# Performance work log

Hardware: AMD Instinct MI355X
Metric: run time of the kernel (lower is better)

Reference implementation:

```python
import jax, jax.numpy as jnp
import numpy as np

B, N = 32, 64
ATTR, STATE, REL, GDIM = 4, 8, 4, 32
NF = 128

def _ln(x, w, b, eps=1e-5):
    mu = jnp.mean(x, axis=-1, keepdims=True)
    var = jnp.mean((x - mu) ** 2, axis=-1, keepdims=True)
    return (x - mu) * jax.lax.rsqrt(var + eps) * w + b

def setup_inputs() -> dict:
    key = jax.random.key(0)
    ks = iter(jax.random.split(key, 32))
    d = {}
    d['attrs'] = jax.random.normal(next(ks), (B, N, ATTR), jnp.float32)
    d['states'] = jax.random.normal(next(ks), (B, N, STATE), jnp.float32)
    d['actions'] = jnp.zeros((B, N, 4), jnp.float32)  # action=False, unused
    d['rel_attrs'] = jax.random.normal(next(ks), (B, N, N, REL), jnp.float32)
    def w(shape):
        return jax.random.normal(next(ks), shape, jnp.float32) * 0.05
    d['oe_w0'] = w((NF, ATTR + STATE)); d['oe_b0'] = jnp.zeros((NF,), jnp.float32)
    d['oe_w1'] = w((NF, NF));            d['oe_b1'] = jnp.zeros((NF,), jnp.float32)
    d['re_w0'] = w((NF, STATE + REL + 2 * ATTR)); d['re_b0'] = jnp.zeros((NF,), jnp.float32)
    d['re_w1'] = w((NF, NF));            d['re_b1'] = jnp.zeros((NF,), jnp.float32)
    d['rp_w'] = w((NF, NF + 2 * NF));    d['rp_b'] = jnp.zeros((NF,), jnp.float32)
    d['rp_lnw'] = jnp.ones((NF,), jnp.float32); d['rp_lnb'] = jnp.zeros((NF,), jnp.float32)
    d['pp_w'] = w((NF, 2 * NF));         d['pp_b'] = jnp.zeros((NF,), jnp.float32)
    d['pp_lnw'] = jnp.ones((NF,), jnp.float32); d['pp_lnb'] = jnp.zeros((NF,), jnp.float32)
    d['pr_w0'] = w((NF, NF));            d['pr_b0'] = jnp.zeros((NF,), jnp.float32)
    d['pr_w1'] = w((GDIM, NF));          d['pr_b1'] = jnp.zeros((GDIM,), jnp.float32)
    d['pstep'] = 2
    return d

def reference(attrs, states, actions, rel_attrs,
              oe_w0, oe_b0, oe_w1, oe_b1,
              re_w0, re_b0, re_w1, re_b1,
              rp_w, rp_b, rp_lnw, rp_lnb,
              pp_w, pp_b, pp_lnw, pp_lnb,
              pr_w0, pr_b0, pr_w1, pr_b1, pstep):
    lin = lambda x, w, b: jnp.einsum('...i,oi->...o', x, w) + b
    # ---- encode nodes: [B,N,attr+state] -> [B,N,NF] (action=False) ----
    obj_in = jnp.concatenate([attrs, states], axis=2)
    obj_encode = jax.nn.relu(lin(jax.nn.relu(lin(obj_in, oe_w0, oe_b0)), oe_w1, oe_b1))
    # ---- encode edges over dense N x N pairs ----
    rel_states = states[:, :, None, :] - states[:, None, :, :]        # B,N,N,state
    recv_attr = jnp.broadcast_to(attrs[:, :, None, :], (attrs.shape[0], attrs.shape[1], attrs.shape[1], attrs.shape[2]))
    send_attr = jnp.broadcast_to(attrs[:, None, :, :], recv_attr.shape)
    rel_in = jnp.concatenate([rel_attrs, rel_states, recv_attr, send_attr], axis=3)
    rel_encode = jax.nn.relu(lin(jax.nn.relu(lin(rel_in, re_w0, re_b0)), re_w1, re_b1))  # B,N,N,NF
    # ---- propagation steps ----
    for _ in range(pstep):
        sh = rel_encode.shape[:3] + (obj_encode.shape[-1],)
        recv = jnp.broadcast_to(obj_encode[:, :, None, :], sh)
        send = jnp.broadcast_to(obj_encode[:, None, :, :], sh)
        rel_effect = jax.nn.relu(_ln(lin(jnp.concatenate([rel_encode, recv, send], axis=3), rp_w, rp_b), rp_lnw, rp_lnb))
        rel_agg = rel_effect.sum(axis=2)                               # B,N,NF
        obj_encode = jax.nn.relu(_ln(lin(jnp.concatenate([obj_encode, rel_agg], axis=2), pp_w, pp_b), pp_lnw, pp_lnb))
    # ---- predict + tanh (state_encoder has tanh=True) ----
    out = lin(jax.nn.relu(lin(obj_encode, pr_w0, pr_b0)), pr_w1, pr_b1)
    return jnp.tanh(out)
```

## Files before the change

kernel.cpp:

```cpp
#include <hip/hip_runtime.h>


#define ROWS 2048
typedef unsigned short u16;
typedef unsigned int u32;
typedef __attribute__((ext_vector_type(8))) short bf16x8;
typedef __attribute__((ext_vector_type(4))) float f32x4;

__device__ __forceinline__ u16 f2b(float f) {
    u32 u = __float_as_uint(f);
    u32 r = (u + 0x7fffu + ((u >> 16) & 1u)) >> 16;
    return (u16)r;
}

__global__ __launch_bounds__(256)
void k_prep(const float* __restrict__ re_w1, const float* __restrict__ rp_w,
            const float* __restrict__ oe_w1, const float* __restrict__ pp_w,
            const float* __restrict__ pr_w0, const float* __restrict__ pr_w1,
            u16* __restrict__ wbfA, u16* __restrict__ wbfB,
            u16* __restrict__ oe_w1b, u16* __restrict__ wrecvb, u16* __restrict__ wsendb,
            u16* __restrict__ pp_wb, u16* __restrict__ pr_w0b, u16* __restrict__ pr_w1b)
{
    int idx = blockIdx.x * 256 + threadIdx.x;
    if (idx < 18432) { int r = idx / 144, c = idx - r * 144;
        wbfA[idx] = f2b(c < 128 ? re_w1[r * 128 + c] : 0.f); return; }
    idx -= 18432;
    if (idx < 18432) { int r = idx / 144, c = idx - r * 144;
        wbfB[idx] = f2b(c < 128 ? rp_w[r * 384 + c] : 0.f); return; }
    idx -= 18432;
    if (idx < 16384) { oe_w1b[idx] = f2b(oe_w1[idx]); return; }
    idx -= 16384;
    if (idx < 16384) { int r = idx >> 7, c = idx & 127;
        wrecvb[idx] = f2b(rp_w[r * 384 + 128 + c]); return; }
    idx -= 16384;
    if (idx < 16384) { int r = idx >> 7, c = idx & 127;
        wsendb[idx] = f2b(rp_w[r * 384 + 256 + c]); return; }
    idx -= 16384;
    if (idx < 32768) { pp_wb[idx] = f2b(pp_w[idx]); return; }
    idx -= 32768;
    if (idx < 16384) { pr_w0b[idx] = f2b(pr_w0[idx]); return; }
    idx -= 16384;
    if (idx < 4096)  { pr_w1b[idx] = f2b(pr_w1[idx]); }
}

__global__ __launch_bounds__(256)
void k_node(const float* __restrict__ attrs, const float* __restrict__ states,
            const float* __restrict__ oe_w0, const float* __restrict__ oe_b0,
            const u16* __restrict__ oe_w1b, const float* __restrict__ oe_b1,
            const float* __restrict__ re_w0, const float* __restrict__ re_b0,
            const u16* __restrict__ wrecvb, const u16* __restrict__ wsendb,
            const float* __restrict__ rp_b,
            u16* __restrict__ objb, float* __restrict__ nr, float* __restrict__ ns,
            float* __restrict__ recvT, float* __restrict__ sendT)
{
    const int r0 = blockIdx.x * 16;
    const int t = threadIdx.x;
    __shared__ float xs[16][12];
    __shared__ float w0s[1536];
    __shared__ float rw0s[2560];
    __shared__ __align__(16) u16 hb[16 * 136];
    __shared__ __align__(16) u16 ob[16 * 136];

    if (t < 192) { int row = t / 12, c = t - row * 12;
        xs[row][c] = (c < 4) ? attrs[(r0 + row) * 4 + c] : states[(r0 + row) * 8 + (c - 4)]; }
    for (int i = t; i < 1536; i += 256) w0s[i] = oe_w0[i];
    for (int i = t; i < 2560; i += 256) rw0s[i] = re_w0[i];
    __syncthreads();

    for (int e = t; e < 2048; e += 256) {
        int row = e >> 7, o = e & 127;
        float h = oe_b0[o];
#pragma unroll
        for (int k = 0; k < 12; k++) h += w0s[o * 12 + k] * xs[row][k];
        hb[row * 136 + o] = f2b(fmaxf(h, 0.f));
        float s0 = 0.f, a0 = 0.f, a1 = 0.f;
#pragma unroll
        for (int k = 0; k < 8; k++) s0 += rw0s[o * 20 + 4 + k] * xs[row][4 + k];
#pragma unroll
        for (int k = 0; k < 4; k++) {
            a0 += rw0s[o * 20 + 12 + k] * xs[row][k];
            a1 += rw0s[o * 20 + 16 + k] * xs[row][k];
        }
        nr[(r0 + row) * 128 + o] = s0 + a0 + re_b0[o];
        ns[(r0 + row) * 128 + o] = a1 - s0;
    }
    __syncthreads();

    const int wave = t >> 6, lane = t & 63, tx = lane & 15, quad = lane >> 4;

    bf16x8 afr[4];
#pragma unroll
    for (int kk = 0; kk < 4; kk++) afr[kk] = *(const bf16x8*)&hb[tx * 136 + kk * 32 + quad * 8];
    f32x4 acc[2]; acc[0] = (f32x4){0.f,0.f,0.f,0.f}; acc[1] = acc[0];
#pragma unroll
    for (int ot = 0; ot < 2; ot++) {
        int o = (wave * 2 + ot) * 16 + tx;
#pragma unroll
        for (int kk = 0; kk < 4; kk++) {
            bf16x8 bfr = *(const bf16x8*)&oe_w1b[o * 128 + kk * 32 + quad * 8];
            acc[ot] = __builtin_amdgcn_mfma_f32_16x16x32_bf16(afr[kk], bfr, acc[ot], 0, 0, 0);
        }
    }
#pragma unroll
    for (int ot = 0; ot < 2; ot++) {
        int o = (wave * 2 + ot) * 16 + tx;
        float bia = oe_b1[o];
#pragma unroll
        for (int r = 0; r < 4; r++)
            ob[(quad * 4 + r) * 136 + o] = f2b(fmaxf(acc[ot][r] + bia, 0.f));
    }
    __syncthreads();
    { int m = t >> 4, c = t & 15;
      *(uint4*)&objb[(r0 + m) * 128 + c * 8] = *(const uint4*)&ob[m * 136 + c * 8]; }

#pragma unroll
    for (int kk = 0; kk < 4; kk++) afr[kk] = *(const bf16x8*)&ob[tx * 136 + kk * 32 + quad * 8];
    f32x4 ar[2], an[2];
    ar[0] = (f32x4){0.f,0.f,0.f,0.f}; ar[1] = ar[0]; an[0] = ar[0]; an[1] = ar[0];
#pragma unroll
    for (int ot = 0; ot < 2; ot++) {
        int o = (wave * 2 + ot) * 16 + tx;
#pragma unroll
        for (int kk = 0; kk < 4; kk++) {
            bf16x8 br = *(const bf16x8*)&wrecvb[o * 128 + kk * 32 + quad * 8];
            ar[ot] = __builtin_amdgcn_mfma_f32_16x16x32_bf16(afr[kk], br, ar[ot], 0, 0, 0);
            bf16x8 bs = *(const bf16x8*)&wsendb[o * 128 + kk * 32 + quad * 8];
            an[ot] = __builtin_amdgcn_mfma_f32_16x16x32_bf16(afr[kk], bs, an[ot], 0, 0, 0);
        }
    }
#pragma unroll
    for (int ot = 0; ot < 2; ot++) {
        int o = (wave * 2 + ot) * 16 + tx;
        float rb = rp_b[o];
#pragma unroll
        for (int r = 0; r < 4; r++) {
            recvT[(r0 + quad * 4 + r) * 128 + o] = ar[ot][r] + rb;
            sendT[(r0 + quad * 4 + r) * 128 + o] = an[ot][r];
        }
    }
}

__global__ __launch_bounds__(256)
void k_edge_enc(const float* __restrict__ rel_attrs,
                const float* __restrict__ re_w0, const u16* __restrict__ wbf,
                const float* __restrict__ re_b1,
                const float* __restrict__ nr, const float* __restrict__ ns,
                u16* __restrict__ relEF)
{
    const int t = threadIdx.x;
    __shared__ __align__(16) u16 wlds[128 * 144];
    __shared__ __align__(16) u16 hsb[64 * 144];
    __shared__ float nrs[128];
    __shared__ float w0a[128][4];
    __shared__ float ras[64][4];

    {
        const uint4* src = (const uint4*)wbf;
        uint4* dst = (uint4*)wlds;
        for (int i = t; i < 2304; i += 256) dst[i] = src[i];
    }
    if (t < 128) {
#pragma unroll
        for (int c = 0; c < 4; c++) w0a[t][c] = re_w0[t * 20 + c];
    }
    const int wave = t >> 6, lane = t & 63, tx = lane & 15, quad = lane >> 4;

    for (int g = 0; g < 4; g++) {
        const int blkg = blockIdx.x * 4 + g;
        const int b = blkg >> 6;
        __syncthreads();
        if (t < 128) nrs[t] = nr[blkg * 128 + t];
        else if (t < 192) {
            int j = t - 128;
#pragma unroll
            for (int c = 0; c < 4; c++) ras[j][c] = rel_attrs[(blkg * 64 + j) * 4 + c];
        }
        __syncthreads();

        for (int e = t; e < 64 * 128; e += 256) {
            int j = e >> 7, o = e & 127;
            float v = nrs[o] + ns[(b * 64 + j) * 128 + o];
#pragma unroll
            for (int c = 0; c < 4; c++) v += w0a[o][c] * ras[j][c];
            hsb[j * 144 + o] = f2b(fmaxf(v, 0.f));
        }
        __syncthreads();

        bf16x8 afr[4];
#pragma unroll
        for (int kk = 0; kk < 4; kk++)
            afr[kk] = *(const bf16x8*)&hsb[(wave * 16 + tx) * 144 + kk * 32 + quad * 8];

        f32x4 acc[8];
#pragma unroll
        for (int oo = 0; oo < 8; oo++) acc[oo] = (f32x4){0.f, 0.f, 0.f, 0.f};
#pragma unroll
        for (int oo = 0; oo < 8; oo++) {
            const int o = oo * 16 + tx;
#pragma unroll
            for (int kk = 0; kk < 4; kk++) {
                bf16x8 bfr = *(const bf16x8*)&wlds[o * 144 + kk * 32 + quad * 8];
                acc[oo] = __builtin_amdgcn_mfma_f32_16x16x32_bf16(afr[kk], bfr, acc[oo], 0, 0, 0);
            }
        }
        __syncthreads();

#pragma unroll
        for (int oo = 0; oo < 8; oo++) {
            const int o = oo * 16 + tx;
            float bia = re_b1[o];
#pragma unroll
            for (int r = 0; r < 4; r++)
                hsb[(wave * 16 + quad * 4 + r) * 144 + o] = f2b(fmaxf(acc[oo][r] + bia, 0.f));
        }
#pragma unroll
        for (int kt = 0; kt < 4; kt++) {
            bf16x8 v = *(const bf16x8*)&hsb[(wave * 16 + tx) * 144 + kt * 32 + quad * 8];
            *(bf16x8*)(relEF + ((size_t)((blkg * 4 + wave) * 4 + kt) * 64 + lane) * 8) = v;
        }
    }
}

__global__ __launch_bounds__(256)
void k_prop_edge(const u16* __restrict__ relEF, const u16* __restrict__ wbf,
                 const float* __restrict__ rp_lnw, const float* __restrict__ rp_lnb,
                 const float* __restrict__ recvT, const float* __restrict__ sendT,
                 u16* __restrict__ aggb)
{
    const int t = threadIdx.x;
    __shared__ __align__(16) u16 wlds[128 * 144];
    __shared__ float scr[16 * 132];
    __shared__ float lnws[128], lnbs[128];

    {
        const uint4* src = (const uint4*)wbf;
        uint4* dst = (uint4*)wlds;
        for (int i = t; i < 2304; i += 256) dst[i] = src[i];
    }
    if (t < 128) { lnws[t] = rp_lnw[t]; lnbs[t] = rp_lnb[t]; }
    __syncthreads();

    const int wave = t >> 6, lane = t & 63, tx = lane & 15, quad = lane >> 4;

    for (int g = 0; g < 4; g++) {
        const int blkg = blockIdx.x * 4 + g;
        const int b = blkg >> 6;

        bf16x8 afr[4];
#pragma unroll
        for (int kt = 0; kt < 4; kt++)
            afr[kt] = *(const bf16x8*)(relEF + ((size_t)((blkg * 4 + wave) * 4 + kt) * 64 + lane) * 8);

        f32x4 acc[8];
#pragma unroll
        for (int oo = 0; oo < 8; oo++) acc[oo] = (f32x4){0.f, 0.f, 0.f, 0.f};
#pragma unroll
        for (int oo = 0; oo < 8; oo++) {
            const int o = oo * 16 + tx;
#pragma unroll
            for (int kk = 0; kk < 4; kk++) {
                bf16x8 bfr = *(const bf16x8*)&wlds[o * 144 + kk * 32 + quad * 8];
                acc[oo] = __builtin_amdgcn_mfma_f32_16x16x32_bf16(afr[kk], bfr, acc[oo], 0, 0, 0);
            }
        }

        const int jrow = wave * 16 + quad * 4;
#pragma unroll
        for (int oo = 0; oo < 8; oo++) {
            const int o = oo * 16 + tx;
            float rv = recvT[blkg * 128 + o];
#pragma unroll
            for (int r = 0; r < 4; r++)
                acc[oo][r] += rv + sendT[(b * 64 + jrow + r) * 128 + o];
        }

        float s[4], q[4];
#pragma unroll
        for (int r = 0; r < 4; r++) {
            s[r] = 0.f; q[r] = 0.f;
#pragma unroll
            for (int oo = 0; oo < 8; oo++) { s[r] += acc[oo][r]; q[r] += acc[oo][r] * acc[oo][r]; }
        }
#pragma unroll
        for (int m = 1; m < 16; m <<= 1) {
#pragma unroll
            for (int r = 0; r < 4; r++) {
                s[r] += __shfl_xor(s[r], m, 64);
                q[r] += __shfl_xor(q[r], m, 64);
            }
        }
        float mu[4], rs[4];
#pragma unroll
        for (int r = 0; r < 4; r++) {
            mu[r] = s[r] * (1.f / 128.f);
            float var = q[r] * (1.f / 128.f) - mu[r] * mu[r];
            rs[r] = rsqrtf(var + 1e-5f);
        }

        float pa[8];
#pragma unroll
        for (int oo = 0; oo < 8; oo++) {
            const int o = oo * 16 + tx;
            float lw = lnws[o], lb = lnbs[o];
            float p = 0.f;
#pragma unroll
            for (int r = 0; r < 4; r++) {
                float z = (acc[oo][r] - mu[r]) * rs[r] * lw + lb;
                p += fmaxf(z, 0.f);
            }
            pa[oo] = p;
        }
        __syncthreads();
        const int grp = wave * 4 + quad;
#pragma unroll
        for (int oo = 0; oo < 8; oo++) scr[grp * 132 + oo * 16 + tx] = pa[oo];
        __syncthreads();
        if (t < 128) {
            float sum = 0.f;
#pragma unroll
            for (int gg = 0; gg < 16; gg++) sum += scr[gg * 132 + t];
            aggb[blkg * 128 + t] = f2b(sum);
        }
    }
}

__global__ __launch_bounds__(256)
void k_prop_node(const u16* __restrict__ aggb,
                 const u16* __restrict__ pp_wb, const float* __restrict__ pp_b,
                 const float* __restrict__ pp_lnw, const float* __restrict__ pp_lnb,
                 const u16* __restrict__ wrecvb, const u16* __restrict__ wsendb,
                 const float* __restrict__ rp_b,
                 u16* __restrict__ objb, float* __restrict__ recvT, float* __restrict__ sendT,
                 int compute_terms)
{
    const int r0 = blockIdx.x * 16;
    const int t = threadIdx.x;
    __shared__ __align__(16) u16 ab[16 * 264];
    __shared__ __align__(16) u16 ob[16 * 136];
    __shared__ float redS[64], redQ[64];

    for (int i = t; i < 512; i += 256) {
        int m = i >> 5, c = i & 31;
        uint4 v = (c < 16) ? *(const uint4*)&objb[(r0 + m) * 128 + (c & 15) * 8]
                           : *(const uint4*)&aggb[(r0 + m) * 128 + (c - 16) * 8];
        *(uint4*)&ab[m * 264 + c * 8] = v;
    }
    __syncthreads();

    const int wave = t >> 6, lane = t & 63, tx = lane & 15, quad = lane >> 4;
    bf16x8 afr[8];
#pragma unroll
    for (int kk = 0; kk < 8; kk++) afr[kk] = *(const bf16x8*)&ab[tx * 264 + kk * 32 + quad * 8];
    f32x4 acc[2]; acc[0] = (f32x4){0.f,0.f,0.f,0.f}; acc[1] = acc[0];
#pragma unroll
    for (int ot = 0; ot < 2; ot++) {
        int o = (wave * 2 + ot) * 16 + tx;
#pragma unroll
        for (int kk = 0; kk < 8; kk++) {
            bf16x8 bfr = *(const bf16x8*)&pp_wb[o * 256 + kk * 32 + quad * 8];
            acc[ot] = __builtin_amdgcn_mfma_f32_16x16x32_bf16(afr[kk], bfr, acc[ot], 0, 0, 0);
        }
    }
#pragma unroll
    for (int ot = 0; ot < 2; ot++) {
        float bia = pp_b[(wave * 2 + ot) * 16 + tx];
#pragma unroll
        for (int r = 0; r < 4; r++) acc[ot][r] += bia;
    }

    float s[4], q[4];
#pragma unroll
    for (int r = 0; r < 4; r++) {
        s[r] = acc[0][r] + acc[1][r];
        q[r] = acc[0][r] * acc[0][r] + acc[1][r] * acc[1][r];
    }
#pragma unroll
    for (int m = 1; m < 16; m <<= 1) {
#pragma unroll
        for (int r = 0; r < 4; r++) {
            s[r] += __shfl_xor(s[r], m, 64);
            q[r] += __shfl_xor(q[r], m, 64);
        }
    }
    if (tx == 0) {
#pragma unroll
        for (int r = 0; r < 4; r++) {
            redS[wave * 16 + quad * 4 + r] = s[r];
            redQ[wave * 16 + quad * 4 + r] = q[r];
        }
    }
    __syncthreads();
    float mu[4], rs[4];
#pragma unroll
    for (int r = 0; r < 4; r++) {
        int m = quad * 4 + r;
        float ss = redS[m] + redS[16 + m] + redS[32 + m] + redS[48 + m];
        float qq = redQ[m] + redQ[16 + m] + redQ[32 + m] + redQ[48 + m];
        mu[r] = ss * (1.f / 128.f);
        rs[r] = rsqrtf(qq * (1.f / 128.f) - mu[r] * mu[r] + 1e-5f);
    }
#pragma unroll
    for (int ot = 0; ot < 2; ot++) {
        int o = (wave * 2 + ot) * 16 + tx;
        float lw = pp_lnw[o], lb = pp_lnb[o];
#pragma unroll
        for (int r = 0; r < 4; r++) {
            float z = (acc[ot][r] - mu[r]) * rs[r] * lw + lb;
            ob[(quad * 4 + r) * 136 + o] = f2b(fmaxf(z, 0.f));
        }
    }
    __syncthreads();
    { int m = t >> 4, c = t & 15;
      *(uint4*)&objb[(r0 + m) * 128 + c * 8] = *(const uint4*)&ob[m * 136 + c * 8]; }

    if (compute_terms) {
        bf16x8 af2[4];
#pragma unroll
        for (int kk = 0; kk < 4; kk++) af2[kk] = *(const bf16x8*)&ob[tx * 136 + kk * 32 + quad * 8];
        f32x4 ar[2], an[2];
        ar[0] = (f32x4){0.f,0.f,0.f,0.f}; ar[1] = ar[0]; an[0] = ar[0]; an[1] = ar[0];
#pragma unroll
        for (int ot = 0; ot < 2; ot++) {
            int o = (wave * 2 + ot) * 16 + tx;
#pragma unroll
            for (int kk = 0; kk < 4; kk++) {
                bf16x8 br = *(const bf16x8*)&wrecvb[o * 128 + kk * 32 + quad * 8];
                ar[ot] = __builtin_amdgcn_mfma_f32_16x16x32_bf16(af2[kk], br, ar[ot], 0, 0, 0);
                bf16x8 bs = *(const bf16x8*)&wsendb[o * 128 + kk * 32 + quad * 8];
                an[ot] = __builtin_amdgcn_mfma_f32_16x16x32_bf16(af2[kk], bs, an[ot], 0, 0, 0);
            }
        }
#pragma unroll
        for (int ot = 0; ot < 2; ot++) {
            int o = (wave * 2 + ot) * 16 + tx;
            float rb = rp_b[o];
#pragma unroll
            for (int r = 0; r < 4; r++) {
                recvT[(r0 + quad * 4 + r) * 128 + o] = ar[ot][r] + rb;
                sendT[(r0 + quad * 4 + r) * 128 + o] = an[ot][r];
            }
        }
    }
}

__global__ __launch_bounds__(256)
void k_predict(const u16* __restrict__ objb,
               const u16* __restrict__ pr_w0b, const float* __restrict__ pr_b0,
               const u16* __restrict__ pr_w1b, const float* __restrict__ pr_b1,
               float* __restrict__ out)
{
    const int r0 = blockIdx.x * 16;
    const int t = threadIdx.x;
    __shared__ __align__(16) u16 ab[16 * 136];
    __shared__ __align__(16) u16 hb2[16 * 136];
    { int m = t >> 4, c = t & 15;
      *(uint4*)&ab[m * 136 + c * 8] = *(const uint4*)&objb[(r0 + m) * 128 + c * 8]; }
    __syncthreads();

    const int wave = t >> 6, lane = t & 63, tx = lane & 15, quad = lane >> 4;
    bf16x8 afr[4];
#pragma unroll
    for (int kk = 0; kk < 4; kk++) afr[kk] = *(const bf16x8*)&ab[tx * 136 + kk * 32 + quad * 8];
    f32x4 acc[2]; acc[0] = (f32x4){0.f,0.f,0.f,0.f}; acc[1] = acc[0];
#pragma unroll
    for (int ot = 0; ot < 2; ot++) {
        int o = (wave * 2 + ot) * 16 + tx;
#pragma unroll
        for (int kk = 0; kk < 4; kk++) {
            bf16x8 bfr = *(const bf16x8*)&pr_w0b[o * 128 + kk * 32 + quad * 8];
            acc[ot] = __builtin_amdgcn_mfma_f32_16x16x32_bf16(afr[kk], bfr, acc[ot], 0, 0, 0);
        }
    }
#pragma unroll
    for (int ot = 0; ot < 2; ot++) {
        int o = (wave * 2 + ot) * 16 + tx;
        float bia = pr_b0[o];
#pragma unroll
        for (int r = 0; r < 4; r++)
            hb2[(quad * 4 + r) * 136 + o] = f2b(fmaxf(acc[ot][r] + bia, 0.f));
    }
    __syncthreads();
    if (wave < 2) {
        bf16x8 af2[4];
#pragma unroll
        for (int kk = 0; kk < 4; kk++) af2[kk] = *(const bf16x8*)&hb2[tx * 136 + kk * 32 + quad * 8];
        f32x4 a2 = (f32x4){0.f,0.f,0.f,0.f};
        int o = wave * 16 + tx;
#pragma unroll
        for (int kk = 0; kk < 4; kk++) {
            bf16x8 bfr = *(const bf16x8*)&pr_w1b[o * 128 + kk * 32 + quad * 8];
            a2 = __builtin_amdgcn_mfma_f32_16x16x32_bf16(af2[kk], bfr, a2, 0, 0, 0);
        }
        float bia = pr_b1[o];
#pragma unroll
        for (int r = 0; r < 4; r++)
            out[(r0 + quad * 4 + r) * 32 + o] = tanhf(a2[r] + bia);
    }
}

extern "C" void kernel_launch(void* const* d_in, const int* in_sizes, int n_in,
                              void* d_out, int out_size, void* d_ws, size_t ws_size,
                              hipStream_t stream)
{
    const float* attrs    = (const float*)d_in[0];
    const float* states   = (const float*)d_in[1];
    const float* rel_attrs= (const float*)d_in[3];
    const float* oe_w0 = (const float*)d_in[4];
    const float* oe_b0 = (const float*)d_in[5];
    const float* oe_w1 = (const float*)d_in[6];
    const float* oe_b1 = (const float*)d_in[7];
    const float* re_w0 = (const float*)d_in[8];
    const float* re_b0 = (const float*)d_in[9];
    const float* re_w1 = (const float*)d_in[10];
    const float* re_b1 = (const float*)d_in[11];
    const float* rp_w  = (const float*)d_in[12];
    const float* rp_b  = (const float*)d_in[13];
    const float* rp_lnw= (const float*)d_in[14];
    const float* rp_lnb= (const float*)d_in[15];
    const float* pp_w  = (const float*)d_in[16];
    const float* pp_b  = (const float*)d_in[17];
    const float* pp_lnw= (const float*)d_in[18];
    const float* pp_lnb= (const float*)d_in[19];
    const float* pr_w0 = (const float*)d_in[20];
    const float* pr_b0 = (const float*)d_in[21];
    const float* pr_w1 = (const float*)d_in[22];
    const float* pr_b1 = (const float*)d_in[23];

    float* ws    = (float*)d_ws;
    float* nr    = ws;
    float* ns    = nr    + ROWS * 128;
    float* recvT = ns    + ROWS * 128;
    float* sendT = recvT + ROWS * 128;
    u16* wbfA   = (u16*)(sendT + ROWS * 128);
    u16* wbfB   = wbfA + 18432;
    u16* oe_w1b = wbfB + 18432;
    u16* wrecvb = oe_w1b + 16384;
    u16* wsendb = wrecvb + 16384;
    u16* pp_wb  = wsendb + 16384;
    u16* pr_w0b = pp_wb + 32768;
    u16* pr_w1b = pr_w0b + 16384;
    u16* objb   = pr_w1b + 4096;
    u16* aggb   = objb + ROWS * 128;
    u16* relEF  = aggb + ROWS * 128;

    k_prep<<<544, 256, 0, stream>>>(re_w1, rp_w, oe_w1, pp_w, pr_w0, pr_w1,
                                    wbfA, wbfB, oe_w1b, wrecvb, wsendb,
                                    pp_wb, pr_w0b, pr_w1b);
    k_node<<<128, 256, 0, stream>>>(attrs, states, oe_w0, oe_b0, oe_w1b, oe_b1,
                                    re_w0, re_b0, wrecvb, wsendb, rp_b,
                                    objb, nr, ns, recvT, sendT);
    k_edge_enc<<<512, 256, 0, stream>>>(rel_attrs, re_w0, wbfA, re_b1, nr, ns, relEF);
    for (int p = 0; p < 2; p++) {
        k_prop_edge<<<512, 256, 0, stream>>>(relEF, wbfB, rp_lnw, rp_lnb, recvT, sendT, aggb);
        k_prop_node<<<128, 256, 0, stream>>>(aggb, pp_wb, pp_b, pp_lnw, pp_lnb,
                                             wrecvb, wsendb, rp_b,
                                             objb, recvT, sendT, (p == 0) ? 1 : 0);
    }
    k_predict<<<128, 256, 0, stream>>>(objb, pr_w0b, pr_b0, pr_w1b, pr_b1, (float*)d_out);
}
```

Measured before the change: 199.6 us.

## Fuse edge encoder with first propagation GEMM and cache rel-effect product

The edge encoder and the first propagation step are merged into one kernel. It computes rel_encode·Wrel in registers and stores that loop-invariant product as bf16, in place of the rel_encode features. The second propagation step then runs a GEMM-free kernel that reads the cached product, adds the recv/send terms, and applies LayerNorm, ReLU and the sum. This removes one kernel launch, one relEF round trip and a repeated 128x128 GEMM over all edges. In exchange, the second step uses a bf16-rounded pre-activation, and the fused kernel reads its second weight matrix straight from global memory instead of LDS.

```diff
diff --git a/kernel.cpp b/kernel.cpp
--- a/kernel.cpp
+++ b/kernel.cpp
@@ -5,8 +5,10 @@
 typedef unsigned short u16;
 typedef unsigned int u32;
 typedef __attribute__((ext_vector_type(8))) short bf16x8;
+typedef __attribute__((ext_vector_type(4))) short bf16x4;
 typedef __attribute__((ext_vector_type(4))) float f32x4;
 
+__device__ __forceinline__ float bsu(u16 u) { return __uint_as_float(((u32)u) << 16); }
 __device__ __forceinline__ u16 f2b(float f) {
     u32 u = __float_as_uint(f);
     u32 r = (u + 0x7fffu + ((u >> 16) & 1u)) >> 16;
@@ -17,17 +19,16 @@
 void k_prep(const float* __restrict__ re_w1, const float* __restrict__ rp_w,
             const float* __restrict__ oe_w1, const float* __restrict__ pp_w,
             const float* __restrict__ pr_w0, const float* __restrict__ pr_w1,
-            u16* __restrict__ wbfA, u16* __restrict__ wbfB,
+            u16* __restrict__ re_w1b, u16* __restrict__ web,
             u16* __restrict__ oe_w1b, u16* __restrict__ wrecvb, u16* __restrict__ wsendb,
             u16* __restrict__ pp_wb, u16* __restrict__ pr_w0b, u16* __restrict__ pr_w1b)
 {
     int idx = blockIdx.x * 256 + threadIdx.x;
-    if (idx < 18432) { int r = idx / 144, c = idx - r * 144;
-        wbfA[idx] = f2b(c < 128 ? re_w1[r * 128 + c] : 0.f); return; }
-    idx -= 18432;
-    if (idx < 18432) { int r = idx / 144, c = idx - r * 144;
-        wbfB[idx] = f2b(c < 128 ? rp_w[r * 384 + c] : 0.f); return; }
-    idx -= 18432;
+    if (idx < 16384) { re_w1b[idx] = f2b(re_w1[idx]); return; }
+    idx -= 16384;
+    if (idx < 16384) { int r = idx >> 7, c = idx & 127;
+        web[idx] = f2b(rp_w[r * 384 + c]); return; }
+    idx -= 16384;
     if (idx < 16384) { oe_w1b[idx] = f2b(oe_w1[idx]); return; }
     idx -= 16384;
     if (idx < 16384) { int r = idx >> 7, c = idx & 127;
@@ -141,11 +142,13 @@
 }
 
 __global__ __launch_bounds__(256)
-void k_edge_enc(const float* __restrict__ rel_attrs,
-                const float* __restrict__ re_w0, const u16* __restrict__ wbf,
-                const float* __restrict__ re_b1,
-                const float* __restrict__ nr, const float* __restrict__ ns,
-                u16* __restrict__ relEF)
+void k_edge_fused(const float* __restrict__ rel_attrs,
+                  const float* __restrict__ re_w0, const u16* __restrict__ re_w1b,
+                  const u16* __restrict__ web, const float* __restrict__ re_b1,
+                  const float* __restrict__ rp_lnw, const float* __restrict__ rp_lnb,
+                  const float* __restrict__ nr, const float* __restrict__ ns,
+                  const float* __restrict__ recvT, const float* __restrict__ sendT,
+                  u16* __restrict__ Ebuf, u16* __restrict__ aggb)
 {
     const int t = threadIdx.x;
     __shared__ __align__(16) u16 wlds[128 * 144];
@@ -153,13 +156,17 @@
     __shared__ float nrs[128];
     __shared__ float w0a[128][4];
     __shared__ float ras[64][4];
+    __shared__ float scr[16 * 132];
+    __shared__ float lnws[128], lnbs[128];
 
     {
-        const uint4* src = (const uint4*)wbf;
-        uint4* dst = (uint4*)wlds;
-        for (int i = t; i < 2304; i += 256) dst[i] = src[i];
+        for (int i = t; i < 2048; i += 256) {
+            int r = i >> 4, c8 = i & 15;
+            *(uint4*)&wlds[r * 144 + c8 * 8] = *(const uint4*)&re_w1b[r * 128 + c8 * 8];
+        }
     }
     if (t < 128) {
+        lnws[t] = rp_lnw[t]; lnbs[t] = rp_lnb[t];
 #pragma unroll
         for (int c = 0; c < 4; c++) w0a[t][c] = re_w0[t * 20 + c];
     }
@@ -190,7 +197,6 @@
 #pragma unroll
         for (int kk = 0; kk < 4; kk++)
             afr[kk] = *(const bf16x8*)&hsb[(wave * 16 + tx) * 144 + kk * 32 + quad * 8];
-
         f32x4 acc[8];
 #pragma unroll
         for (int oo = 0; oo < 8; oo++) acc[oo] = (f32x4){0.f, 0.f, 0.f, 0.f};
@@ -203,8 +209,6 @@
                 acc[oo] = __builtin_amdgcn_mfma_f32_16x16x32_bf16(afr[kk], bfr, acc[oo], 0, 0, 0);
             }
         }
-        __syncthreads();
-
 #pragma unroll
         for (int oo = 0; oo < 8; oo++) {
             const int o = oo * 16 + tx;
@@ -213,55 +217,29 @@
             for (int r = 0; r < 4; r++)
                 hsb[(wave * 16 + quad * 4 + r) * 144 + o] = f2b(fmaxf(acc[oo][r] + bia, 0.f));
         }
-#pragma unroll
-        for (int kt = 0; kt < 4; kt++) {
-            bf16x8 v = *(const bf16x8*)&hsb[(wave * 16 + tx) * 144 + kt * 32 + quad * 8];
-            *(bf16x8*)(relEF + ((size_t)((blkg * 4 + wave) * 4 + kt) * 64 + lane) * 8) = v;
-        }
-    }
-}
-
-__global__ __launch_bounds__(256)
-void k_prop_edge(const u16* __restrict__ relEF, const u16* __restrict__ wbf,
-                 const float* __restrict__ rp_lnw, const float* __restrict__ rp_lnb,
-                 const float* __restrict__ recvT, const float* __restrict__ sendT,
-                 u16* __restrict__ aggb)
-{
-    const int t = threadIdx.x;
-    __shared__ __align__(16) u16 wlds[128 * 144];
-    __shared__ float scr[16 * 132];
-    __shared__ float lnws[128], lnbs[128];
-
-    {
-        const uint4* src = (const uint4*)wbf;
-        uint4* dst = (uint4*)wlds;
-        for (int i = t; i < 2304; i += 256) dst[i] = src[i];
-    }
-    if (t < 128) { lnws[t] = rp_lnw[t]; lnbs[t] = rp_lnb[t]; }
-    __syncthreads();
-
-    const int wave = t >> 6, lane = t & 63, tx = lane & 15, quad = lane >> 4;
-
-    for (int g = 0; g < 4; g++) {
-        const int blkg = blockIdx.x * 4 + g;
-        const int b = blkg >> 6;
-
-        bf16x8 afr[4];
-#pragma unroll
-        for (int kt = 0; kt < 4; kt++)
-            afr[kt] = *(const bf16x8*)(relEF + ((size_t)((blkg * 4 + wave) * 4 + kt) * 64 + lane) * 8);
-
-        f32x4 acc[8];
-#pragma unroll
-        for (int oo = 0; oo < 8; oo++) acc[oo] = (f32x4){0.f, 0.f, 0.f, 0.f};
+        bf16x8 af2[4];
+#pragma unroll
+        for (int kk = 0; kk < 4; kk++)
+            af2[kk] = *(const bf16x8*)&hsb[(wave * 16 + tx) * 144 + kk * 32 + quad * 8];
+        f32x4 acc2[8];
+#pragma unroll
+        for (int oo = 0; oo < 8; oo++) acc2[oo] = (f32x4){0.f, 0.f, 0.f, 0.f};
 #pragma unroll
         for (int oo = 0; oo < 8; oo++) {
-            const int o = oo * 16 + tx;
+            const int o2 = oo * 16 + tx;
 #pragma unroll
             for (int kk = 0; kk < 4; kk++) {
-                bf16x8 bfr = *(const bf16x8*)&wlds[o * 144 + kk * 32 + quad * 8];
-                acc[oo] = __builtin_amdgcn_mfma_f32_16x16x32_bf16(afr[kk], bfr, acc[oo], 0, 0, 0);
+                bf16x8 bfr = *(const bf16x8*)&web[o2 * 128 + kk * 32 + quad * 8];
+                acc2[oo] = __builtin_amdgcn_mfma_f32_16x16x32_bf16(af2[kk], bfr, acc2[oo], 0, 0, 0);
             }
+        }
+        const int tid = blkg * 4 + wave;
+#pragma unroll
+        for (int oo = 0; oo < 8; oo++) {
+            bf16x4 v;
+            v[0] = (short)f2b(acc2[oo][0]); v[1] = (short)f2b(acc2[oo][1]);
+            v[2] = (short)f2b(acc2[oo][2]); v[3] = (short)f2b(acc2[oo][3]);
+            *(bf16x4*)(Ebuf + ((size_t)(tid * 8 + oo) * 64 + lane) * 4) = v;
         }
 
         const int jrow = wave * 16 + quad * 4;
@@ -271,15 +249,14 @@
             float rv = recvT[blkg * 128 + o];
 #pragma unroll
             for (int r = 0; r < 4; r++)
-                acc[oo][r] += rv + sendT[(b * 64 + jrow + r) * 128 + o];
-        }
-
+                acc2[oo][r] += rv + sendT[(b * 64 + jrow + r) * 128 + o];
+        }
         float s[4], q[4];
 #pragma unroll
         for (int r = 0; r < 4; r++) {
             s[r] = 0.f; q[r] = 0.f;
 #pragma unroll
-            for (int oo = 0; oo < 8; oo++) { s[r] += acc[oo][r]; q[r] += acc[oo][r] * acc[oo][r]; }
+            for (int oo = 0; oo < 8; oo++) { s[r] += acc2[oo][r]; q[r] += acc2[oo][r] * acc2[oo][r]; }
         }
 #pragma unroll
         for (int m = 1; m < 16; m <<= 1) {
@@ -296,7 +273,6 @@
             float var = q[r] * (1.f / 128.f) - mu[r] * mu[r];
             rs[r] = rsqrtf(var + 1e-5f);
         }
-
         float pa[8];
 #pragma unroll
         for (int oo = 0; oo < 8; oo++) {
@@ -305,7 +281,7 @@
             float p = 0.f;
 #pragma unroll
             for (int r = 0; r < 4; r++) {
-                float z = (acc[oo][r] - mu[r]) * rs[r] * lw + lb;
+                float z = (acc2[oo][r] - mu[r]) * rs[r] * lw + lb;
                 p += fmaxf(z, 0.f);
             }
             pa[oo] = p;
@@ -321,6 +297,80 @@
             for (int gg = 0; gg < 16; gg++) sum += scr[gg * 132 + t];
             aggb[blkg * 128 + t] = f2b(sum);
         }
+    }
+}
+
+__global__ __launch_bounds__(256)
+void k_prop_edge2(const u16* __restrict__ Ebuf,
+                  const float* __restrict__ rp_lnw, const float* __restrict__ rp_lnb,
+                  const float* __restrict__ recvT, const float* __restrict__ sendT,
+                  u16* __restrict__ aggb)
+{
+    const int blk = blockIdx.x;
+    const int b = blk >> 6;
+    const int t = threadIdx.x;
+    __shared__ float scr[16 * 132];
+    __shared__ float lnws[128], lnbs[128];
+    if (t < 128) { lnws[t] = rp_lnw[t]; lnbs[t] = rp_lnb[t]; }
+    __syncthreads();
+
+    const int wave = t >> 6, lane = t & 63, tx = lane & 15, quad = lane >> 4;
+    const int tid = blk * 4 + wave;
+    const int jrow = wave * 16 + quad * 4;
+
+    float y[8][4];
+#pragma unroll
+    for (int oo = 0; oo < 8; oo++) {
+        bf16x4 v = *(const bf16x4*)(Ebuf + ((size_t)(tid * 8 + oo) * 64 + lane) * 4);
+        const int o = oo * 16 + tx;
+        float rv = recvT[blk * 128 + o];
+#pragma unroll
+        for (int r = 0; r < 4; r++)
+            y[oo][r] = bsu((u16)v[r]) + rv + sendT[(b * 64 + jrow + r) * 128 + o];
+    }
+    float s[4], q[4];
+#pragma unroll
+    for (int r = 0; r < 4; r++) {
+        s[r] = 0.f; q[r] = 0.f;
+#pragma unroll
+        for (int oo = 0; oo < 8; oo++) { s[r] += y[oo][r]; q[r] += y[oo][r] * y[oo][r]; }
+    }
+#pragma unroll
+    for (int m = 1; m < 16; m <<= 1) {
+#pragma unroll
+        for (int r = 0; r < 4; r++) {
+            s[r] += __shfl_xor(s[r], m, 64);
+            q[r] += __shfl_xor(q[r], m, 64);
+        }
+    }
+    float mu[4], rs[4];
+#pragma unroll
+    for (int r = 0; r < 4; r++) {
+        mu[r] = s[r] * (1.f / 128.f);
+        rs[r] = rsqrtf(q[r] * (1.f / 128.f) - mu[r] * mu[r] + 1e-5f);
+    }
+    float pa[8];
+#pragma unroll
+    for (int oo = 0; oo < 8; oo++) {
+        const int o = oo * 16 + tx;
+        float lw = lnws[o], lb = lnbs[o];
+        float p = 0.f;
+#pragma unroll
+        for (int r = 0; r < 4; r++) {
+            float z = (y[oo][r] - mu[r]) * rs[r] * lw + lb;
+            p += fmaxf(z, 0.f);
+        }
+        pa[oo] = p;
+    }
+    const int grp = wave * 4 + quad;
+#pragma unroll
+    for (int oo = 0; oo < 8; oo++) scr[grp * 132 + oo * 16 + tx] = pa[oo];
+    __syncthreads();
+    if (t < 128) {
+        float sum = 0.f;
+#pragma unroll
+        for (int gg = 0; gg < 16; gg++) sum += scr[gg * 132 + t];
+        aggb[blk * 128 + t] = f2b(sum);
     }
 }
 
@@ -531,30 +581,33 @@
     float* ns    = nr    + ROWS * 128;
     float* recvT = ns    + ROWS * 128;
     float* sendT = recvT + ROWS * 128;
-    u16* wbfA   = (u16*)(sendT + ROWS * 128);
-    u16* wbfB   = wbfA + 18432;
-    u16* oe_w1b = wbfB + 18432;
+    u16* re_w1b = (u16*)(sendT + ROWS * 128);
+    u16* web    = re_w1b + 16384;
+    u16* oe_w1b = web    + 16384;
     u16* wrecvb = oe_w1b + 16384;
     u16* wsendb = wrecvb + 16384;
     u16* pp_wb  = wsendb + 16384;
-    u16* pr_w0b = pp_wb + 32768;
+    u16* pr_w0b = pp_wb  + 32768;
     u16* pr_w1b = pr_w0b + 16384;
     u16* objb   = pr_w1b + 4096;
     u16* aggb   = objb + ROWS * 128;
-    u16* relEF  = aggb + ROWS * 128;
-
-    k_prep<<<544, 256, 0, stream>>>(re_w1, rp_w, oe_w1, pp_w, pr_w0, pr_w1,
-                                    wbfA, wbfB, oe_w1b, wrecvb, wsendb,
+    u16* Ebuf   = aggb + ROWS * 128;
+
+    k_prep<<<528, 256, 0, stream>>>(re_w1, rp_w, oe_w1, pp_w, pr_w0, pr_w1,
+                                    re_w1b, web, oe_w1b, wrecvb, wsendb,
                                     pp_wb, pr_w0b, pr_w1b);
     k_node<<<128, 256, 0, stream>>>(attrs, states, oe_w0, oe_b0, oe_w1b, oe_b1,
                                     re_w0, re_b0, wrecvb, wsendb, rp_b,
                                     objb, nr, ns, recvT, sendT);
-    k_edge_enc<<<512, 256, 0, stream>>>(rel_attrs, re_w0, wbfA, re_b1, nr, ns, relEF);
-    for (int p = 0; p < 2; p++) {
-        k_prop_edge<<<512, 256, 0, stream>>>(relEF, wbfB, rp_lnw, rp_lnb, recvT, sendT, aggb);
-        k_prop_node<<<128, 256, 0, stream>>>(aggb, pp_wb, pp_b, pp_lnw, pp_lnb,
-                                             wrecvb, wsendb, rp_b,
-                                             objb, recvT, sendT, (p == 0) ? 1 : 0);
-    }
+    k_edge_fused<<<512, 256, 0, stream>>>(rel_attrs, re_w0, re_w1b, web, re_b1,
+                                          rp_lnw, rp_lnb, nr, ns, recvT, sendT,
+                                          Ebuf, aggb);
+    k_prop_node<<<128, 256, 0, stream>>>(aggb, pp_wb, pp_b, pp_lnw, pp_lnb,
+                                         wrecvb, wsendb, rp_b,
+                                         objb, recvT, sendT, 1);
+    k_prop_edge2<<<2048, 256, 0, stream>>>(Ebuf, rp_lnw, rp_lnb, recvT, sendT, aggb);
+    k_prop_node<<<128, 256, 0, stream>>>(aggb, pp_wb, pp_b, pp_lnw, pp_lnb,
+                                         wrecvb, wsendb, rp_b,
+                                         objb, recvT, sendT, 0);
     k_predict<<<128, 256, 0, stream>>>(objb, pr_w0b, pr_b0, pr_w1b, pr_b1, (float*)d_out);
 }
```

New measurement: 204.2 us. +2.3%, slower.
